# Optimization experiments

Hardware: AMD Instinct MI355X
Metric: run time of the kernel (lower is better)

## Reference

```python
import jax, jax.numpy as jnp
import numpy as np

EMB = 512
H1, H2 = 300, 100


def setup_inputs() -> dict:
    key = jax.random.key(0)
    ks = jax.random.split(key, 12)
    B, N, M = 2, 256, 256
    inp = {
        "action_embedding": jax.random.normal(ks[0], (B, EMB, N), jnp.float32),
        "anchor_embedding": jax.random.normal(ks[1], (B, EMB, M), jnp.float32),
        "action_points": jax.random.normal(ks[2], (B, 3, N), jnp.float32),
        "anchor_points": jax.random.normal(ks[3], (B, 3, M), jnp.float32),
        # MLPKernel params: Linear(1024,300), Linear(300,100), Linear(100,1), stored as [in,out]
        "W1": jax.random.normal(ks[4], (2 * EMB, H1), jnp.float32) / np.sqrt(2 * EMB),
        "b1": jax.random.normal(ks[5], (H1,), jnp.float32) * 0.01,
        "W2": jax.random.normal(ks[6], (H1, H2), jnp.float32) / np.sqrt(H1),
        "b2": jax.random.normal(ks[7], (H2,), jnp.float32) * 0.01,
        "W3": jax.random.normal(ks[8], (H2, 1), jnp.float32) / np.sqrt(H2),
        "b3": jax.random.normal(ks[9], (1,), jnp.float32) * 0.01,
    }
    return inp


def _pairwise_radii(Phi_A, Phi_B, W1, b1, W2, b2, W3, b3):
    # MLPKernel: softplus((mlp(cat(a,b)) + mlp(cat(b,a))) / 2) over all (n, m) pairs.
    # Split first linear: cat(x1,x2) @ W1 == x1 @ Wa + x2 @ Wb  (no [B,N,M,1024] materialization).
    F = Phi_A.shape[-1]
    Wa, Wb = W1[:F], W1[F:]
    hA_a = jnp.einsum('bnf,fh->bnh', Phi_A, Wa)
    hA_b = jnp.einsum('bnf,fh->bnh', Phi_A, Wb)
    hB_a = jnp.einsum('bmf,fh->bmh', Phi_B, Wa)
    hB_b = jnp.einsum('bmf,fh->bmh', Phi_B, Wb)

    def mlp_rest(h):  # h: [B,N,M,H1] pre-bias first-layer activations
        h = jax.nn.relu(h + b1)
        h = jax.nn.relu(jnp.einsum('bnmh,hk->bnmk', h, W2) + b2)
        return jnp.einsum('bnmk,ko->bnmo', h, W3) + b3

    v1 = mlp_rest(hA_a[:, :, None, :] + hB_b[:, None, :, :])  # mlp(cat(A_n, B_m))
    v2 = mlp_rest(hB_a[:, None, :, :] + hA_b[:, :, None, :])  # mlp(cat(B_m, A_n))
    return jax.nn.softplus((v1 + v2) * 0.5)[..., 0]  # [B,N,M]


def _multilaterate(P, R, W):
    # Vectorized estimate_p over batch b and query point n.
    # P: [B,M,3] anchor points, R: [B,N,M] estimated radii, W: [B,M] weights.
    M = P.shape[1]
    norm2 = jnp.sum(P * P, axis=-1)                      # [B,M]  (Pt @ P)
    d = norm2[:, None, :] - R ** 2                       # [B,N,M]  PtP - r^2
    a = jnp.einsum('bm,bnm,bmd->bnd', W, d, P) / M       # [B,N,3]
    WPPt = jnp.einsum('bm,bmd,bme->bde', W, P, P) / M    # [B,3,3]  mean(W * P Pt)
    mWd = jnp.einsum('bm,bnm->bn', W, d) / M             # [B,N]    mean(W * (PtP - r^2))
    c = jnp.einsum('bm,bmd->bd', W, P) / M               # [B,3]
    # B @ c with B = -2*mean(W*PPt) - mean(W*d)*I
    Bc = -2.0 * jnp.einsum('bde,be->bd', WPPt, c)[:, None, :] - mWd[..., None] * c[:, None, :]
    cc = jnp.sum(c * c, axis=-1)                         # [B]
    f = a + Bc + 2.0 * cc[:, None, None] * c[:, None, :]  # [B,N,3]
    PPt_mean = jnp.einsum('bmd,bme->bde', P, P) / M       # unweighted mean(PPt)
    H = -2.0 * PPt_mean + 2.0 * jnp.einsum('bd,be->bde', c, c)  # [B,3,3]
    Hinv = jnp.linalg.inv(H)
    q = -jnp.einsum('bde,bne->bnd', Hinv, f)
    return q + c[:, None, :]                              # [B,N,3]


def reference(action_embedding, anchor_embedding, action_points, anchor_points,
              W1, b1, W2, b2, W3, b3):
    P_A = jnp.transpose(action_points, (0, 2, 1))    # [B,N,3]
    P_B = jnp.transpose(anchor_points, (0, 2, 1))    # [B,M,3]
    Phi_A = jnp.transpose(action_embedding, (0, 2, 1))  # [B,N,F]
    Phi_B = jnp.transpose(anchor_embedding, (0, 2, 1))  # [B,M,F]
    B_weights = jnp.ones(Phi_B.shape[:2], dtype=Phi_B.dtype)
    R_est = _pairwise_radii(Phi_A, Phi_B, W1, b1, W2, b2, W3, b3)
    P_A_B_pred = _multilaterate(P_B, R_est, B_weights)  # [B,N,3]
    flow = jnp.transpose(P_A_B_pred - P_A, (0, 2, 1))   # [B,3,N] == full_flow (pred_weight=False)
    return flow
```

## Files before the change

kernel.cpp:

```cpp
#include <hip/hip_runtime.h>
#include <math.h>

#define EMB 512
#define H1 300
#define H2 100
#define NB 2
#define NN 256
#define MM 256

#define OFF_HAA 0
#define OFF_HAB (OFF_HAA + NB*NN*H1)
#define OFF_HBA (OFF_HAB + NB*NN*H1)
#define OFF_HBB (OFF_HBA + NB*NN*H1)
#define OFF_S   (OFF_HBB + NB*NN*H1)
#define OFF_CST (OFF_S + NB*NN*4)
#define OFF_W2C (OFF_CST + 64)
#define OFF_B2P (OFF_W2C + 17920)
#define OFF_W3P (OFF_B2P + 112)

typedef __attribute__((ext_vector_type(8))) short bf16x8;
typedef __attribute__((ext_vector_type(4))) float f32x4;

static __device__ inline unsigned f2bfbits(float f) {
    union { float f; unsigned u; } v; v.f = f;
    return (v.u + 0x7fffu + ((v.u >> 16) & 1u)) >> 16;
}

__global__ void k_prep(const float* __restrict__ W2, const float* __restrict__ b2,
                       const float* __restrict__ W3, float* __restrict__ ws)
{
    unsigned short* W2c = (unsigned short*)(ws + OFF_W2C);
    int start = blockIdx.x * 256 + threadIdx.x;
    for (int idx = start; idx < 10*112*32; idx += gridDim.x * 256) {
        int c  = idx / 3584;
        int r  = idx - c * 3584;
        int j  = r >> 5;
        int kk = r & 31;
        int k  = c * 32 + kk;
        float v = (j < H2 && k < H1) ? W2[k * H2 + j] : 0.0f;
        W2c[idx] = (unsigned short)f2bfbits(v);
    }
    if (blockIdx.x == 0 && threadIdx.x < 112) {
        int j = threadIdx.x;
        ws[OFF_B2P + j] = (j < H2) ? b2[j] : 0.0f;
        ws[OFF_W3P + j] = (j < H2) ? W3[j] : 0.0f;
    }
}

__global__ void k_const(const float* __restrict__ anchor_pts, float* __restrict__ cst)
{
    int b = blockIdx.x;
    int m = threadIdx.x;
    float px = anchor_pts[b*3*MM + 0*MM + m];
    float py = anchor_pts[b*3*MM + 1*MM + m];
    float pz = anchor_pts[b*3*MM + 2*MM + m];
    float n2 = px*px + py*py + pz*pz;

    float v[13];
    v[0]=px; v[1]=py; v[2]=pz;
    v[3]=px*px; v[4]=px*py; v[5]=px*pz; v[6]=py*py; v[7]=py*pz; v[8]=pz*pz;
    v[9]=n2*px; v[10]=n2*py; v[11]=n2*pz; v[12]=n2;

    #pragma unroll
    for (int off = 32; off >= 1; off >>= 1) {
        #pragma unroll
        for (int i = 0; i < 13; i++) v[i] += __shfl_xor(v[i], off, 64);
    }
    __shared__ float red[4][13];
    int wave = threadIdx.x >> 6, lane = threadIdx.x & 63;
    if (lane == 0) {
        #pragma unroll
        for (int i = 0; i < 13; i++) red[wave][i] = v[i];
    }
    __syncthreads();
    if (threadIdx.x == 0) {
        float s[13];
        #pragma unroll
        for (int i = 0; i < 13; i++)
            s[i] = red[0][i] + red[1][i] + red[2][i] + red[3][i];
        const float invM = 1.0f / MM;
        float c0 = s[0]*invM, c1 = s[1]*invM, c2 = s[2]*invM;
        float Pxx = s[3]*invM, Pxy = s[4]*invM, Pxz = s[5]*invM;
        float Pyy = s[6]*invM, Pyz = s[7]*invM, Pzz = s[8]*invM;

        float H00 = -2.0f*Pxx + 2.0f*c0*c0;
        float H01 = -2.0f*Pxy + 2.0f*c0*c1;
        float H02 = -2.0f*Pxz + 2.0f*c0*c2;
        float H11 = -2.0f*Pyy + 2.0f*c1*c1;
        float H12 = -2.0f*Pyz + 2.0f*c1*c2;
        float H22 = -2.0f*Pzz + 2.0f*c2*c2;
        float H10 = H01, H20 = H02, H21 = H12;

        float det = H00*(H11*H22 - H12*H21)
                  - H01*(H10*H22 - H12*H20)
                  + H02*(H10*H21 - H11*H20);
        float id = 1.0f / det;
        float i00 = (H11*H22 - H12*H21)*id;
        float i01 = (H02*H21 - H01*H22)*id;
        float i02 = (H01*H12 - H02*H11)*id;
        float i10 = (H12*H20 - H10*H22)*id;
        float i11 = (H00*H22 - H02*H20)*id;
        float i12 = (H02*H10 - H00*H12)*id;
        float i20 = (H10*H21 - H11*H20)*id;
        float i21 = (H01*H20 - H00*H21)*id;
        float i22 = (H00*H11 - H01*H10)*id;

        float t0x = -2.0f*(Pxx*c0 + Pxy*c1 + Pxz*c2);
        float t0y = -2.0f*(Pxy*c0 + Pyy*c1 + Pyz*c2);
        float t0z = -2.0f*(Pxz*c0 + Pyz*c1 + Pzz*c2);
        float cc = c0*c0 + c1*c1 + c2*c2;

        float* C = cst + b*32;
        C[0]=c0; C[1]=c1; C[2]=c2;
        C[3]=i00; C[4]=i01; C[5]=i02;
        C[6]=i10; C[7]=i11; C[8]=i12;
        C[9]=i20; C[10]=i21; C[11]=i22;
        C[12]=t0x; C[13]=t0y; C[14]=t0z;
        C[15]=cc;
        C[16]=s[9]*invM; C[17]=s[10]*invM; C[18]=s[11]*invM; C[19]=s[12]*invM;
    }
}

#define BN 64
#define BH 32
#define BK 32

__global__ __launch_bounds__(256) void k_hidden(
    const float* __restrict__ actE, const float* __restrict__ ancE,
    const float* __restrict__ W1, const float* __restrict__ b1,
    float* __restrict__ ws)
{
    int bs = blockIdx.z;
    int b = bs >> 1, src = bs & 1;
    int n0 = blockIdx.x * BN;
    int h0 = blockIdx.y * BH;
    const float* E = (src == 0 ? actE : ancE) + b * EMB * NN;
    float* outA = ws + (src == 0 ? OFF_HAA : OFF_HBA) + b * NN * H1;
    float* outB = ws + (src == 0 ? OFF_HAB : OFF_HBB) + b * NN * H1;

    __shared__ float Elds[BK][BN];
    __shared__ float Wlds[BK][BH];

    int tid = threadIdx.x;
    int tx = tid & 15;
    int ty = tid >> 4;

    float acc[4][2];
    #pragma unroll
    for (int i = 0; i < 4; i++) { acc[i][0] = 0.0f; acc[i][1] = 0.0f; }

    int ek  = tid >> 4;
    int en4 = (tid & 15) * 4;
    int wk  = tid >> 3;
    int wh4 = (tid & 7) * 4;
    int gh  = h0 + wh4;
    bool wvalid = (gh < 600);
    int whalf = (gh >= 300) ? 1 : 0;
    const float* wsrc = W1 + (size_t)whalf * EMB * H1 + (gh - whalf * 300);

    for (int k0 = 0; k0 < EMB; k0 += BK) {
        float4 e0 = *(const float4*)&E[(k0 + ek) * NN + n0 + en4];
        float4 e1 = *(const float4*)&E[(k0 + ek + 16) * NN + n0 + en4];
        float4 wv = make_float4(0.f, 0.f, 0.f, 0.f);
        if (wvalid) wv = *(const float4*)&wsrc[(size_t)(k0 + wk) * H1];

        __syncthreads();
        *(float4*)&Elds[ek][en4]      = e0;
        *(float4*)&Elds[ek + 16][en4] = e1;
        *(float4*)&Wlds[wk][wh4]      = wv;
        __syncthreads();

        #pragma unroll
        for (int k = 0; k < BK; k++) {
            float4 ev = *(const float4*)&Elds[k][ty * 4];
            float2 wv2 = *(const float2*)&Wlds[k][tx * 2];
            acc[0][0] = fmaf(ev.x, wv2.x, acc[0][0]);
            acc[0][1] = fmaf(ev.x, wv2.y, acc[0][1]);
            acc[1][0] = fmaf(ev.y, wv2.x, acc[1][0]);
            acc[1][1] = fmaf(ev.y, wv2.y, acc[1][1]);
            acc[2][0] = fmaf(ev.z, wv2.x, acc[2][0]);
            acc[2][1] = fmaf(ev.z, wv2.y, acc[2][1]);
            acc[3][0] = fmaf(ev.w, wv2.x, acc[3][0]);
            acc[3][1] = fmaf(ev.w, wv2.y, acc[3][1]);
        }
    }

    #pragma unroll
    for (int i = 0; i < 4; i++) {
        int n = n0 + ty * 4 + i;
        #pragma unroll
        for (int j = 0; j < 2; j++) {
            int h = h0 + tx * 2 + j;
            if (h < 600) {
                int hh = (h < 300) ? h : h - 300;
                float bias = (src == 0) ? b1[hh] : 0.0f;
                float val = acc[i][j] + bias;
                if (h < 300) outA[n * H1 + hh] = val;
                else         outB[n * H1 + hh] = val;
            }
        }
    }
}

__global__ __launch_bounds__(256, 2) void k_pair(
    const float* __restrict__ ws_f,
    const float* __restrict__ ancP,
    float* __restrict__ S)
{
    int b  = blockIdx.z;
    int n0 = blockIdx.y * 16, m0 = blockIdx.x * 16;
    int tid = threadIdx.x;
    int lane = tid & 63, w = tid >> 6;
    int colj = lane & 15;
    int quad = lane >> 4;

    __shared__ float hAfL[16 * 36];
    __shared__ float hBfL[16 * 36];
    __shared__ short Abf[256 * 40];
    __shared__ short W2L[112 * 40];

    const unsigned short* W2c = (const unsigned short*)(ws_f + OFF_W2C);
    const float* b2p = ws_f + OFF_B2P;
    const float* w3p = ws_f + OFF_W3P;

    float b2v[7], w3v[7];
    #pragma unroll
    for (int jt = 0; jt < 7; jt++) {
        b2v[jt] = b2p[jt * 16 + colj];
        w3v[jt] = w3p[jt * 16 + colj];
    }
    float pxv[4], pyv[4], pzv[4];
    #pragma unroll
    for (int r = 0; r < 4; r++) {
        int m = m0 + quad * 4 + r;
        pxv[r] = ancP[b*3*MM + 0*MM + m];
        pyv[r] = ancP[b*3*MM + 1*MM + m];
        pzv[r] = ancP[b*3*MM + 2*MM + m];
    }

    const float* Xb[2] = { ws_f + OFF_HAA + (size_t)(b*NN + n0) * H1,
                           ws_f + OFF_HAB + (size_t)(b*NN + n0) * H1 };
    const float* Yb[2] = { ws_f + OFF_HBB + (size_t)(b*NN + m0) * H1,
                           ws_f + OFF_HBA + (size_t)(b*NN + m0) * H1 };

    int sarr = tid >> 7;
    int srow = (tid >> 3) & 15;
    int sseg = tid & 7;
    int nl = tid >> 4, ml = tid & 15;

    float vsum[4][4];
    #pragma unroll
    for (int i = 0; i < 4; i++)
        #pragma unroll
        for (int r = 0; r < 4; r++) vsum[i][r] = 0.0f;

    #pragma unroll
    for (int p = 0; p < 2; p++) {
        f32x4 acc[4][7];
        #pragma unroll
        for (int i = 0; i < 4; i++)
            #pragma unroll
            for (int jt = 0; jt < 7; jt++)
                acc[i][jt] = (f32x4){0.f, 0.f, 0.f, 0.f};

        const float* Xp = Xb[p];
        const float* Yp = Yb[p];
        const float* ssrc = (sarr ? Yp : Xp) + srow * H1;

        for (int c = 0; c < 10; c++) {
            int k0 = c * 32;
            float4 sv = *(const float4*)&ssrc[k0 + sseg * 4];
            const uint4* wsrc4 = (const uint4*)W2c + c * 448;
            uint4 w0 = wsrc4[tid];
            uint4 w1 = wsrc4[(tid + 256) % 448];

            __syncthreads();
            {
                float* dst = (sarr ? hBfL : hAfL) + srow * 36 + sseg * 4;
                *(float4*)dst = sv;
            }
            {
                int j = tid >> 2, q = tid & 3;
                *(uint4*)&W2L[j * 40 + q * 8] = w0;
                if (tid < 192) {
                    int u2 = tid + 256;
                    int j2 = u2 >> 2, q2 = u2 & 3;
                    *(uint4*)&W2L[j2 * 40 + q2 * 8] = w1;
                }
            }
            __syncthreads();

            {
                const float* xa = hAfL + nl * 36;
                const float* xb = hBfL + ml * 36;
                short* arow = Abf + tid * 40;
                #pragma unroll
                for (int sg = 0; sg < 4; sg++) {
                    float4 a0 = *(const float4*)&xa[sg * 8];
                    float4 a1 = *(const float4*)&xa[sg * 8 + 4];
                    float4 c0 = *(const float4*)&xb[sg * 8];
                    float4 c1 = *(const float4*)&xb[sg * 8 + 4];
                    float h0 = fmaxf(a0.x + c0.x, 0.f);
                    float h1 = fmaxf(a0.y + c0.y, 0.f);
                    float h2 = fmaxf(a0.z + c0.z, 0.f);
                    float h3 = fmaxf(a0.w + c0.w, 0.f);
                    float h4 = fmaxf(a1.x + c1.x, 0.f);
                    float h5 = fmaxf(a1.y + c1.y, 0.f);
                    float h6 = fmaxf(a1.z + c1.z, 0.f);
                    float h7 = fmaxf(a1.w + c1.w, 0.f);
                    uint4 pk;
                    pk.x = f2bfbits(h0) | (f2bfbits(h1) << 16);
                    pk.y = f2bfbits(h2) | (f2bfbits(h3) << 16);
                    pk.z = f2bfbits(h4) | (f2bfbits(h5) << 16);
                    pk.w = f2bfbits(h6) | (f2bfbits(h7) << 16);
                    *(uint4*)&arow[sg * 8] = pk;
                }
            }
            __syncthreads();

            int koff = quad * 8;
            bf16x8 bfr[7];
            #pragma unroll
            for (int jt = 0; jt < 7; jt++)
                bfr[jt] = *(const bf16x8*)&W2L[(jt * 16 + colj) * 40 + koff];
            #pragma unroll
            for (int i = 0; i < 4; i++) {
                int pr = (w * 4 + i) * 16 + colj;
                bf16x8 af = *(const bf16x8*)&Abf[pr * 40 + koff];
                #pragma unroll
                for (int jt = 0; jt < 7; jt++)
                    acc[i][jt] = __builtin_amdgcn_mfma_f32_16x16x32_bf16(
                        af, bfr[jt], acc[i][jt], 0, 0, 0);
            }
        }

        #pragma unroll
        for (int i = 0; i < 4; i++)
            #pragma unroll
            for (int jt = 0; jt < 7; jt++)
                #pragma unroll
                for (int r = 0; r < 4; r++)
                    vsum[i][r] = fmaf(fmaxf(acc[i][jt][r] + b2v[jt], 0.f),
                                      w3v[jt], vsum[i][r]);
    }

    #pragma unroll
    for (int i = 0; i < 4; i++)
        #pragma unroll
        for (int r = 0; r < 4; r++) {
            float v = vsum[i][r];
            v += __shfl_xor(v, 1, 16);
            v += __shfl_xor(v, 2, 16);
            v += __shfl_xor(v, 4, 16);
            v += __shfl_xor(v, 8, 16);
            vsum[i][r] = v;
        }

    #pragma unroll
    for (int i = 0; i < 4; i++) {
        float s0 = 0.f, s1 = 0.f, s2 = 0.f, s3 = 0.f;
        #pragma unroll
        for (int r = 0; r < 4; r++) {
            float x = 0.5f * vsum[i][r];
            float R = fmaxf(x, 0.f) + log1pf(expf(-fabsf(x)));
            float r2 = R * R;
            s0 = fmaf(r2, pxv[r], s0);
            s1 = fmaf(r2, pyv[r], s1);
            s2 = fmaf(r2, pzv[r], s2);
            s3 += r2;
        }
        s0 += __shfl_xor(s0, 16, 64); s0 += __shfl_xor(s0, 32, 64);
        s1 += __shfl_xor(s1, 16, 64); s1 += __shfl_xor(s1, 32, 64);
        s2 += __shfl_xor(s2, 16, 64); s2 += __shfl_xor(s2, 32, 64);
        s3 += __shfl_xor(s3, 16, 64); s3 += __shfl_xor(s3, 32, 64);
        if (lane == 0) {
            int n = n0 + w * 4 + i;
            float* sp = S + (b*NN + n) * 4;
            atomicAdd(sp + 0, s0);
            atomicAdd(sp + 1, s1);
            atomicAdd(sp + 2, s2);
            atomicAdd(sp + 3, s3);
        }
    }
}

__global__ void k_final(const float* __restrict__ S, const float* __restrict__ cst,
                        const float* __restrict__ action_pts, float* __restrict__ out)
{
    int b = blockIdx.x;
    int n = threadIdx.x;
    const float* C = cst + b*32;
    float c0=C[0], c1=C[1], c2=C[2];
    float t0x=C[12], t0y=C[13], t0z=C[14];
    float cc=C[15];
    float SnP0=C[16], SnP1=C[17], SnP2=C[18], Sn=C[19];

    const float* sp = S + (b*NN + n) * 4;
    const float invM = 1.0f / MM;
    float a0 = SnP0 - sp[0]*invM;
    float a1 = SnP1 - sp[1]*invM;
    float a2 = SnP2 - sp[2]*invM;
    float mWd = Sn - sp[3]*invM;

    float f0 = a0 + t0x - mWd*c0 + 2.0f*cc*c0;
    float f1 = a1 + t0y - mWd*c1 + 2.0f*cc*c1;
    float f2 = a2 + t0z - mWd*c2 + 2.0f*cc*c2;

    float q0 = -(C[3]*f0 + C[4]*f1 + C[5]*f2);
    float q1 = -(C[6]*f0 + C[7]*f1 + C[8]*f2);
    float q2 = -(C[9]*f0 + C[10]*f1 + C[11]*f2);

    float p0 = q0 + c0, p1 = q1 + c1, p2 = q2 + c2;

    out[b*3*NN + 0*NN + n] = p0 - action_pts[b*3*NN + 0*NN + n];
    out[b*3*NN + 1*NN + n] = p1 - action_pts[b*3*NN + 1*NN + n];
    out[b*3*NN + 2*NN + n] = p2 - action_pts[b*3*NN + 2*NN + n];
}

extern "C" void kernel_launch(void* const* d_in, const int* in_sizes, int n_in,
                              void* d_out, int out_size, void* d_ws, size_t ws_size,
                              hipStream_t stream)
{
    const float* actE = (const float*)d_in[0];
    const float* ancE = (const float*)d_in[1];
    const float* actP = (const float*)d_in[2];
    const float* ancP = (const float*)d_in[3];
    const float* W1   = (const float*)d_in[4];
    const float* b1   = (const float*)d_in[5];
    const float* W2   = (const float*)d_in[6];
    const float* b2   = (const float*)d_in[7];
    const float* W3   = (const float*)d_in[8];
    const float* b3   = (const float*)d_in[9];
    float* ws  = (float*)d_ws;
    float* out = (float*)d_out;

    hipMemsetAsync(ws + OFF_S, 0, NB*NN*4*sizeof(float), stream);
    k_prep<<<16, 256, 0, stream>>>(W2, b2, W3, ws);
    k_const<<<NB, 256, 0, stream>>>(ancP, ws + OFF_CST);
    k_hidden<<<dim3(4, 19, 4), 256, 0, stream>>>(actE, ancE, W1, b1, ws);
    k_pair<<<dim3(16, 16, NB), 256, 0, stream>>>(ws, ancP, ws + OFF_S);
    k_final<<<NB, 256, 0, stream>>>(ws + OFF_S, ws + OFF_CST, actP, out);
}
```

Baseline: 155.6 us.

## Use bf16 MFMA for first layer, split pair kernel by permutation, add reduction kernel

Adds transpose-and-convert kernels for W1 and the embeddings to bf16, so the first-layer GEMM runs on MFMA instead of fp32 FMAs. The pair kernel is split across the two MLP permutations as separate grid slices. It builds the bf16 A-fragment directly in registers instead of staging it through shared memory, which removes an LDS buffer and a barrier. Per-pair logits are written to a workspace buffer and a new reduction kernel applies softplus and accumulates the multilateration sums, replacing the atomics and the memset. This adds kernel launches and extra global traffic, and lowers first-layer precision to bf16.

New measurement: 132.5 us. 1.17x faster.

```diff
diff --git a/kernel.cpp b/kernel.cpp
--- a/kernel.cpp
+++ b/kernel.cpp
@@ -1,4 +1,5 @@
 #include <hip/hip_runtime.h>
+#include <hip/hip_bf16.h>
 #include <math.h>
 
 #define EMB 512
@@ -9,14 +10,17 @@
 #define MM 256
 
 #define OFF_HAA 0
-#define OFF_HAB (OFF_HAA + NB*NN*H1)
-#define OFF_HBA (OFF_HAB + NB*NN*H1)
-#define OFF_HBB (OFF_HBA + NB*NN*H1)
-#define OFF_S   (OFF_HBB + NB*NN*H1)
-#define OFF_CST (OFF_S + NB*NN*4)
-#define OFF_W2C (OFF_CST + 64)
-#define OFF_B2P (OFF_W2C + 17920)
-#define OFF_W3P (OFF_B2P + 112)
+#define OFF_HAB 153600
+#define OFF_HBA 307200
+#define OFF_HBB 460800
+#define OFF_S   614400
+#define OFF_CST 616448
+#define OFF_W2C 616512
+#define OFF_B2P 634432
+#define OFF_W3P 634544
+#define OFF_ET  634656
+#define OFF_W1T 896800
+#define OFF_V   1060640
 
 typedef __attribute__((ext_vector_type(8))) short bf16x8;
 typedef __attribute__((ext_vector_type(4))) float f32x4;
@@ -24,6 +28,11 @@
 static __device__ inline unsigned f2bfbits(float f) {
     union { float f; unsigned u; } v; v.f = f;
     return (v.u + 0x7fffu + ((v.u >> 16) & 1u)) >> 16;
+}
+static __device__ inline unsigned pack_bf2(float a, float b) {
+    union { __hip_bfloat162 h; unsigned u; } cv;
+    cv.h = __float22bfloat162_rn(make_float2(a, b));
+    return cv.u;
 }
 
 __global__ void k_prep(const float* __restrict__ W2, const float* __restrict__ b2,
@@ -45,6 +54,53 @@
         ws[OFF_B2P + j] = (j < H2) ? b2[j] : 0.0f;
         ws[OFF_W3P + j] = (j < H2) ? W3[j] : 0.0f;
     }
+}
+
+__global__ void k_prepw1(const float* __restrict__ W1, float* __restrict__ ws)
+{
+    __shared__ float Tf[32 * 36];
+    unsigned short* W1t = (unsigned short*)(ws + OFF_W1T);
+    int h0 = blockIdx.x * 32, f0 = blockIdx.y * 32;
+    int tid = threadIdx.x;
+    int fr = tid >> 3, hc4 = (tid & 7) * 4;
+    int hg = h0 + hc4;
+    float4 v = make_float4(0.f, 0.f, 0.f, 0.f);
+    if (hg < 600) {
+        int half = (hg >= 300) ? 1 : 0;
+        int hh = hg - half * 300;
+        v = *(const float4*)&W1[(size_t)(half * EMB + f0 + fr) * H1 + hh];
+    }
+    *(float4*)&Tf[fr * 36 + hc4] = v;
+    __syncthreads();
+    int hr = tid >> 3, f4 = (tid & 7) * 4;
+    float v0 = Tf[(f4 + 0) * 36 + hr];
+    float v1 = Tf[(f4 + 1) * 36 + hr];
+    float v2 = Tf[(f4 + 2) * 36 + hr];
+    float v3 = Tf[(f4 + 3) * 36 + hr];
+    uint2 pk = make_uint2(pack_bf2(v0, v1), pack_bf2(v2, v3));
+    *(uint2*)&W1t[(size_t)(h0 + hr) * EMB + f0 + f4] = pk;
+}
+
+__global__ void k_prepe(const float* __restrict__ actE, const float* __restrict__ ancE,
+                        float* __restrict__ ws)
+{
+    __shared__ float Tf[32 * 36];
+    unsigned short* Et = (unsigned short*)(ws + OFF_ET);
+    int f0 = blockIdx.x * 32, n0 = blockIdx.y * 32;
+    int bs = blockIdx.z, b = bs >> 1, src = bs & 1;
+    const float* E = (src == 0 ? actE : ancE) + (size_t)b * EMB * NN;
+    int tid = threadIdx.x;
+    int r = tid >> 3, c4 = (tid & 7) * 4;
+    float4 v = *(const float4*)&E[(size_t)(f0 + r) * NN + n0 + c4];
+    *(float4*)&Tf[r * 36 + c4] = v;
+    __syncthreads();
+    int nr = tid >> 3, f4 = (tid & 7) * 4;
+    float v0 = Tf[(f4 + 0) * 36 + nr];
+    float v1 = Tf[(f4 + 1) * 36 + nr];
+    float v2 = Tf[(f4 + 2) * 36 + nr];
+    float v3 = Tf[(f4 + 3) * 36 + nr];
+    uint2 pk = make_uint2(pack_bf2(v0, v1), pack_bf2(v2, v3));
+    *(uint2*)&Et[((size_t)(bs * NN) + n0 + nr) * EMB + f0 + f4] = pk;
 }
 
 __global__ void k_const(const float* __restrict__ anchor_pts, float* __restrict__ cst)
@@ -121,228 +177,158 @@
     }
 }
 
-#define BN 64
-#define BH 32
-#define BK 32
-
 __global__ __launch_bounds__(256) void k_hidden(
-    const float* __restrict__ actE, const float* __restrict__ ancE,
-    const float* __restrict__ W1, const float* __restrict__ b1,
-    float* __restrict__ ws)
-{
-    int bs = blockIdx.z;
-    int b = bs >> 1, src = bs & 1;
-    int n0 = blockIdx.x * BN;
-    int h0 = blockIdx.y * BH;
-    const float* E = (src == 0 ? actE : ancE) + b * EMB * NN;
-    float* outA = ws + (src == 0 ? OFF_HAA : OFF_HBA) + b * NN * H1;
-    float* outB = ws + (src == 0 ? OFF_HAB : OFF_HBB) + b * NN * H1;
-
-    __shared__ float Elds[BK][BN];
-    __shared__ float Wlds[BK][BH];
+    float* __restrict__ ws, const float* __restrict__ b1)
+{
+    int bs = blockIdx.z, b = bs >> 1, src = bs & 1;
+    int n0 = blockIdx.x * 32;
+    int h0 = blockIdx.y * 64;
+    const unsigned short* Et  = (const unsigned short*)(ws + OFF_ET)
+                                + (size_t)(bs * NN) * EMB;
+    const unsigned short* W1t = (const unsigned short*)(ws + OFF_W1T);
+    float* outA = ws + (src == 0 ? OFF_HAA : OFF_HBA) + (size_t)b * NN * H1;
+    float* outB = ws + (src == 0 ? OFF_HAB : OFF_HBB) + (size_t)b * NN * H1;
+
+    __shared__ unsigned short EtL[32 * 40];
+    __shared__ unsigned short W1tL[64 * 40];
 
     int tid = threadIdx.x;
-    int tx = tid & 15;
-    int ty = tid >> 4;
-
-    float acc[4][2];
-    #pragma unroll
-    for (int i = 0; i < 4; i++) { acc[i][0] = 0.0f; acc[i][1] = 0.0f; }
-
-    int ek  = tid >> 4;
-    int en4 = (tid & 15) * 4;
-    int wk  = tid >> 3;
-    int wh4 = (tid & 7) * 4;
-    int gh  = h0 + wh4;
-    bool wvalid = (gh < 600);
-    int whalf = (gh >= 300) ? 1 : 0;
-    const float* wsrc = W1 + (size_t)whalf * EMB * H1 + (gh - whalf * 300);
-
-    for (int k0 = 0; k0 < EMB; k0 += BK) {
-        float4 e0 = *(const float4*)&E[(k0 + ek) * NN + n0 + en4];
-        float4 e1 = *(const float4*)&E[(k0 + ek + 16) * NN + n0 + en4];
-        float4 wv = make_float4(0.f, 0.f, 0.f, 0.f);
-        if (wvalid) wv = *(const float4*)&wsrc[(size_t)(k0 + wk) * H1];
-
+    int lane = tid & 63, w = tid >> 6;
+    int colj = lane & 15, quad = lane >> 4;
+    int pt = w & 1, jt0 = (w >> 1) * 2;
+
+    int erow = tid >> 3, es4 = (tid & 7) * 4;
+    int wrow = tid >> 2, ws8 = (tid & 3) * 8;
+
+    f32x4 acc[2];
+    acc[0] = (f32x4){0.f,0.f,0.f,0.f};
+    acc[1] = (f32x4){0.f,0.f,0.f,0.f};
+
+    for (int c = 0; c < 16; c++) {
+        int k0 = c * 32;
+        uint2 ev = *(const uint2*)&Et[(size_t)(n0 + erow) * EMB + k0 + es4];
+        uint4 wv = *(const uint4*)&W1t[(size_t)(h0 + wrow) * EMB + k0 + ws8];
         __syncthreads();
-        *(float4*)&Elds[ek][en4]      = e0;
-        *(float4*)&Elds[ek + 16][en4] = e1;
-        *(float4*)&Wlds[wk][wh4]      = wv;
+        *(uint2*)&EtL[erow * 40 + es4] = ev;
+        *(uint4*)&W1tL[wrow * 40 + ws8] = wv;
         __syncthreads();
 
-        #pragma unroll
-        for (int k = 0; k < BK; k++) {
-            float4 ev = *(const float4*)&Elds[k][ty * 4];
-            float2 wv2 = *(const float2*)&Wlds[k][tx * 2];
-            acc[0][0] = fmaf(ev.x, wv2.x, acc[0][0]);
-            acc[0][1] = fmaf(ev.x, wv2.y, acc[0][1]);
-            acc[1][0] = fmaf(ev.y, wv2.x, acc[1][0]);
-            acc[1][1] = fmaf(ev.y, wv2.y, acc[1][1]);
-            acc[2][0] = fmaf(ev.z, wv2.x, acc[2][0]);
-            acc[2][1] = fmaf(ev.z, wv2.y, acc[2][1]);
-            acc[3][0] = fmaf(ev.w, wv2.x, acc[3][0]);
-            acc[3][1] = fmaf(ev.w, wv2.y, acc[3][1]);
+        bf16x8 af  = *(const bf16x8*)&EtL[(pt * 16 + colj) * 40 + quad * 8];
+        bf16x8 bf0 = *(const bf16x8*)&W1tL[(jt0 * 16 + colj) * 40 + quad * 8];
+        bf16x8 bf1 = *(const bf16x8*)&W1tL[((jt0 + 1) * 16 + colj) * 40 + quad * 8];
+        acc[0] = __builtin_amdgcn_mfma_f32_16x16x32_bf16(af, bf0, acc[0], 0, 0, 0);
+        acc[1] = __builtin_amdgcn_mfma_f32_16x16x32_bf16(af, bf1, acc[1], 0, 0, 0);
+    }
+
+    #pragma unroll
+    for (int j2 = 0; j2 < 2; j2++) {
+        int hg = h0 + (jt0 + j2) * 16 + colj;
+        if (hg >= 600) continue;
+        int hh = (hg < 300) ? hg : hg - 300;
+        float* o = (hg < 300) ? outA : outB;
+        float bias = (src == 0) ? b1[hh] : 0.0f;
+        #pragma unroll
+        for (int r = 0; r < 4; r++) {
+            int n = n0 + pt * 16 + quad * 4 + r;
+            o[(size_t)n * H1 + hh] = acc[j2][r] + bias;
         }
     }
-
-    #pragma unroll
-    for (int i = 0; i < 4; i++) {
-        int n = n0 + ty * 4 + i;
-        #pragma unroll
-        for (int j = 0; j < 2; j++) {
-            int h = h0 + tx * 2 + j;
-            if (h < 600) {
-                int hh = (h < 300) ? h : h - 300;
-                float bias = (src == 0) ? b1[hh] : 0.0f;
-                float val = acc[i][j] + bias;
-                if (h < 300) outA[n * H1 + hh] = val;
-                else         outB[n * H1 + hh] = val;
-            }
-        }
-    }
-}
-
-__global__ __launch_bounds__(256, 2) void k_pair(
-    const float* __restrict__ ws_f,
-    const float* __restrict__ ancP,
-    float* __restrict__ S)
-{
-    int b  = blockIdx.z;
+}
+
+__global__ __launch_bounds__(256) void k_pair(
+    const float* __restrict__ ws_f, const float* __restrict__ b3p,
+    float* __restrict__ V)
+{
+    int bz = blockIdx.z, b = bz >> 1, p = bz & 1;
     int n0 = blockIdx.y * 16, m0 = blockIdx.x * 16;
     int tid = threadIdx.x;
     int lane = tid & 63, w = tid >> 6;
-    int colj = lane & 15;
-    int quad = lane >> 4;
+    int colj = lane & 15, quad = lane >> 4;
 
     __shared__ float hAfL[16 * 36];
     __shared__ float hBfL[16 * 36];
-    __shared__ short Abf[256 * 40];
     __shared__ short W2L[112 * 40];
 
     const unsigned short* W2c = (const unsigned short*)(ws_f + OFF_W2C);
-    const float* b2p = ws_f + OFF_B2P;
-    const float* w3p = ws_f + OFF_W3P;
-
     float b2v[7], w3v[7];
     #pragma unroll
     for (int jt = 0; jt < 7; jt++) {
-        b2v[jt] = b2p[jt * 16 + colj];
-        w3v[jt] = w3p[jt * 16 + colj];
-    }
-    float pxv[4], pyv[4], pzv[4];
-    #pragma unroll
-    for (int r = 0; r < 4; r++) {
-        int m = m0 + quad * 4 + r;
-        pxv[r] = ancP[b*3*MM + 0*MM + m];
-        pyv[r] = ancP[b*3*MM + 1*MM + m];
-        pzv[r] = ancP[b*3*MM + 2*MM + m];
-    }
-
-    const float* Xb[2] = { ws_f + OFF_HAA + (size_t)(b*NN + n0) * H1,
-                           ws_f + OFF_HAB + (size_t)(b*NN + n0) * H1 };
-    const float* Yb[2] = { ws_f + OFF_HBB + (size_t)(b*NN + m0) * H1,
-                           ws_f + OFF_HBA + (size_t)(b*NN + m0) * H1 };
+        b2v[jt] = ws_f[OFF_B2P + jt * 16 + colj];
+        w3v[jt] = ws_f[OFF_W3P + jt * 16 + colj];
+    }
+    float b3val = b3p[0];
+
+    const float* srcX = ws_f + (p == 0 ? OFF_HAA : OFF_HAB) + (size_t)(b*NN + n0) * H1;
+    const float* srcY = ws_f + (p == 0 ? OFF_HBB : OFF_HBA) + (size_t)(b*NN + m0) * H1;
 
     int sarr = tid >> 7;
     int srow = (tid >> 3) & 15;
     int sseg = tid & 7;
-    int nl = tid >> 4, ml = tid & 15;
-
-    float vsum[4][4];
+    const float* ssrc = (sarr ? srcY : srcX) + srow * H1;
+    float* sdst = (sarr ? hBfL : hAfL) + srow * 36 + sseg * 4;
+
+    f32x4 acc[4][7];
     #pragma unroll
     for (int i = 0; i < 4; i++)
         #pragma unroll
-        for (int r = 0; r < 4; r++) vsum[i][r] = 0.0f;
-
-    #pragma unroll
-    for (int p = 0; p < 2; p++) {
-        f32x4 acc[4][7];
-        #pragma unroll
-        for (int i = 0; i < 4; i++)
+        for (int jt = 0; jt < 7; jt++)
+            acc[i][jt] = (f32x4){0.f,0.f,0.f,0.f};
+
+    for (int c = 0; c < 10; c++) {
+        float4 sv = *(const float4*)&ssrc[c * 32 + sseg * 4];
+        const uint4* wsrc4 = (const uint4*)W2c + c * 448;
+        uint4 w0 = wsrc4[tid];
+        uint4 w1 = wsrc4[(tid + 256) % 448];
+
+        __syncthreads();
+        *(float4*)sdst = sv;
+        {
+            int j = tid >> 2, q = tid & 3;
+            *(uint4*)&W2L[j * 40 + q * 8] = w0;
+            if (tid < 192) {
+                int u2 = tid + 256;
+                *(uint4*)&W2L[(u2 >> 2) * 40 + (u2 & 3) * 8] = w1;
+            }
+        }
+        __syncthreads();
+
+        float4 hb0 = *(const float4*)&hBfL[colj * 36 + quad * 8];
+        float4 hb1 = *(const float4*)&hBfL[colj * 36 + quad * 8 + 4];
+        bf16x8 bfr[7];
+        #pragma unroll
+        for (int jt = 0; jt < 7; jt++)
+            bfr[jt] = *(const bf16x8*)&W2L[(jt * 16 + colj) * 40 + quad * 8];
+
+        #pragma unroll
+        for (int i = 0; i < 4; i++) {
+            const float* xa = &hAfL[(w * 4 + i) * 36 + quad * 8];
+            float4 ha0 = *(const float4*)&xa[0];
+            float4 ha1 = *(const float4*)&xa[4];
+            union { unsigned u[4]; bf16x8 v; } af;
+            af.u[0] = pack_bf2(fmaxf(ha0.x + hb0.x, 0.f), fmaxf(ha0.y + hb0.y, 0.f));
+            af.u[1] = pack_bf2(fmaxf(ha0.z + hb0.z, 0.f), fmaxf(ha0.w + hb0.w, 0.f));
+            af.u[2] = pack_bf2(fmaxf(ha1.x + hb1.x, 0.f), fmaxf(ha1.y + hb1.y, 0.f));
+            af.u[3] = pack_bf2(fmaxf(ha1.z + hb1.z, 0.f), fmaxf(ha1.w + hb1.w, 0.f));
             #pragma unroll
             for (int jt = 0; jt < 7; jt++)
-                acc[i][jt] = (f32x4){0.f, 0.f, 0.f, 0.f};
-
-        const float* Xp = Xb[p];
-        const float* Yp = Yb[p];
-        const float* ssrc = (sarr ? Yp : Xp) + srow * H1;
-
-        for (int c = 0; c < 10; c++) {
-            int k0 = c * 32;
-            float4 sv = *(const float4*)&ssrc[k0 + sseg * 4];
-            const uint4* wsrc4 = (const uint4*)W2c + c * 448;
-            uint4 w0 = wsrc4[tid];
-            uint4 w1 = wsrc4[(tid + 256) % 448];
-
-            __syncthreads();
-            {
-                float* dst = (sarr ? hBfL : hAfL) + srow * 36 + sseg * 4;
-                *(float4*)dst = sv;
-            }
-            {
-                int j = tid >> 2, q = tid & 3;
-                *(uint4*)&W2L[j * 40 + q * 8] = w0;
-                if (tid < 192) {
-                    int u2 = tid + 256;
-                    int j2 = u2 >> 2, q2 = u2 & 3;
-                    *(uint4*)&W2L[j2 * 40 + q2 * 8] = w1;
-                }
-            }
-            __syncthreads();
-
-            {
-                const float* xa = hAfL + nl * 36;
-                const float* xb = hBfL + ml * 36;
-                short* arow = Abf + tid * 40;
-                #pragma unroll
-                for (int sg = 0; sg < 4; sg++) {
-                    float4 a0 = *(const float4*)&xa[sg * 8];
-                    float4 a1 = *(const float4*)&xa[sg * 8 + 4];
-                    float4 c0 = *(const float4*)&xb[sg * 8];
-                    float4 c1 = *(const float4*)&xb[sg * 8 + 4];
-                    float h0 = fmaxf(a0.x + c0.x, 0.f);
-                    float h1 = fmaxf(a0.y + c0.y, 0.f);
-                    float h2 = fmaxf(a0.z + c0.z, 0.f);
-                    float h3 = fmaxf(a0.w + c0.w, 0.f);
-                    float h4 = fmaxf(a1.x + c1.x, 0.f);
-                    float h5 = fmaxf(a1.y + c1.y, 0.f);
-                    float h6 = fmaxf(a1.z + c1.z, 0.f);
-                    float h7 = fmaxf(a1.w + c1.w, 0.f);
-                    uint4 pk;
-                    pk.x = f2bfbits(h0) | (f2bfbits(h1) << 16);
-                    pk.y = f2bfbits(h2) | (f2bfbits(h3) << 16);
-                    pk.z = f2bfbits(h4) | (f2bfbits(h5) << 16);
-                    pk.w = f2bfbits(h6) | (f2bfbits(h7) << 16);
-                    *(uint4*)&arow[sg * 8] = pk;
-                }
-            }
-            __syncthreads();
-
-            int koff = quad * 8;
-            bf16x8 bfr[7];
+                acc[i][jt] = __builtin_amdgcn_mfma_f32_16x16x32_bf16(
+                    af.v, bfr[jt], acc[i][jt], 0, 0, 0);
+        }
+    }
+
+    float vsum[4][4];
+    #pragma unroll
+    for (int i = 0; i < 4; i++)
+        #pragma unroll
+        for (int r = 0; r < 4; r++) vsum[i][r] = 0.0f;
+    #pragma unroll
+    for (int i = 0; i < 4; i++)
+        #pragma unroll
+        for (int jt = 0; jt < 7; jt++)
             #pragma unroll
-            for (int jt = 0; jt < 7; jt++)
-                bfr[jt] = *(const bf16x8*)&W2L[(jt * 16 + colj) * 40 + koff];
-            #pragma unroll
-            for (int i = 0; i < 4; i++) {
-                int pr = (w * 4 + i) * 16 + colj;
-                bf16x8 af = *(const bf16x8*)&Abf[pr * 40 + koff];
-                #pragma unroll
-                for (int jt = 0; jt < 7; jt++)
-                    acc[i][jt] = __builtin_amdgcn_mfma_f32_16x16x32_bf16(
-                        af, bfr[jt], acc[i][jt], 0, 0, 0);
-            }
-        }
-
-        #pragma unroll
-        for (int i = 0; i < 4; i++)
-            #pragma unroll
-            for (int jt = 0; jt < 7; jt++)
-                #pragma unroll
-                for (int r = 0; r < 4; r++)
-                    vsum[i][r] = fmaf(fmaxf(acc[i][jt][r] + b2v[jt], 0.f),
-                                      w3v[jt], vsum[i][r]);
-    }
+            for (int r = 0; r < 4; r++)
+                vsum[i][r] = fmaf(fmaxf(acc[i][jt][r] + b2v[jt], 0.f),
+                                  w3v[jt], vsum[i][r]);
 
     #pragma unroll
     for (int i = 0; i < 4; i++)
@@ -356,31 +342,53 @@
             vsum[i][r] = v;
         }
 
-    #pragma unroll
-    for (int i = 0; i < 4; i++) {
-        float s0 = 0.f, s1 = 0.f, s2 = 0.f, s3 = 0.f;
-        #pragma unroll
-        for (int r = 0; r < 4; r++) {
-            float x = 0.5f * vsum[i][r];
-            float R = fmaxf(x, 0.f) + log1pf(expf(-fabsf(x)));
-            float r2 = R * R;
-            s0 = fmaf(r2, pxv[r], s0);
-            s1 = fmaf(r2, pyv[r], s1);
-            s2 = fmaf(r2, pzv[r], s2);
-            s3 += r2;
+    if (colj == 0) {
+        #pragma unroll
+        for (int i = 0; i < 4; i++) {
+            int n = n0 + w * 4 + i;
+            float4 o;
+            o.x = 0.5f * (vsum[i][0] + b3val);
+            o.y = 0.5f * (vsum[i][1] + b3val);
+            o.z = 0.5f * (vsum[i][2] + b3val);
+            o.w = 0.5f * (vsum[i][3] + b3val);
+            *(float4*)&V[(((size_t)p * NB + b) * NN + n) * MM + m0 + quad * 4] = o;
         }
-        s0 += __shfl_xor(s0, 16, 64); s0 += __shfl_xor(s0, 32, 64);
-        s1 += __shfl_xor(s1, 16, 64); s1 += __shfl_xor(s1, 32, 64);
-        s2 += __shfl_xor(s2, 16, 64); s2 += __shfl_xor(s2, 32, 64);
-        s3 += __shfl_xor(s3, 16, 64); s3 += __shfl_xor(s3, 32, 64);
-        if (lane == 0) {
-            int n = n0 + w * 4 + i;
-            float* sp = S + (b*NN + n) * 4;
-            atomicAdd(sp + 0, s0);
-            atomicAdd(sp + 1, s1);
-            atomicAdd(sp + 2, s2);
-            atomicAdd(sp + 3, s3);
-        }
+    }
+}
+
+__global__ void k_red(const float* __restrict__ V, const float* __restrict__ ancP,
+                      float* __restrict__ S)
+{
+    int b = blockIdx.y;
+    int n = blockIdx.x * 16 + (threadIdx.x >> 4);
+    int ml = threadIdx.x & 15;
+    const float* v0 = V + (((size_t)0 * NB + b) * NN + n) * MM;
+    const float* v1 = V + (((size_t)1 * NB + b) * NN + n) * MM;
+    float s0 = 0.f, s1 = 0.f, s2 = 0.f, s3 = 0.f;
+    #pragma unroll
+    for (int k = 0; k < 16; k++) {
+        int m = ml + k * 16;
+        float x = v0[m] + v1[m];
+        float R = fmaxf(x, 0.f) + log1pf(expf(-fabsf(x)));
+        float r2 = R * R;
+        float px = ancP[b*3*MM + 0*MM + m];
+        float py = ancP[b*3*MM + 1*MM + m];
+        float pz = ancP[b*3*MM + 2*MM + m];
+        s0 = fmaf(r2, px, s0);
+        s1 = fmaf(r2, py, s1);
+        s2 = fmaf(r2, pz, s2);
+        s3 += r2;
+    }
+    #pragma unroll
+    for (int off = 8; off >= 1; off >>= 1) {
+        s0 += __shfl_xor(s0, off, 16);
+        s1 += __shfl_xor(s1, off, 16);
+        s2 += __shfl_xor(s2, off, 16);
+        s3 += __shfl_xor(s3, off, 16);
+    }
+    if (ml == 0) {
+        float4 o = make_float4(s0, s1, s2, s3);
+        *(float4*)&S[(size_t)(b * NN + n) * 4] = o;
     }
 }
 
@@ -434,10 +442,12 @@
     float* ws  = (float*)d_ws;
     float* out = (float*)d_out;
 
-    hipMemsetAsync(ws + OFF_S, 0, NB*NN*4*sizeof(float), stream);
-    k_prep<<<16, 256, 0, stream>>>(W2, b2, W3, ws);
-    k_const<<<NB, 256, 0, stream>>>(ancP, ws + OFF_CST);
-    k_hidden<<<dim3(4, 19, 4), 256, 0, stream>>>(actE, ancE, W1, b1, ws);
-    k_pair<<<dim3(16, 16, NB), 256, 0, stream>>>(ws, ancP, ws + OFF_S);
-    k_final<<<NB, 256, 0, stream>>>(ws + OFF_S, ws + OFF_CST, actP, out);
-}
+    k_prep  <<<16, 256, 0, stream>>>(W2, b2, W3, ws);
+    k_prepw1<<<dim3(20, 16), 256, 0, stream>>>(W1, ws);
+    k_prepe <<<dim3(16, 8, 4), 256, 0, stream>>>(actE, ancE, ws);
+    k_const <<<NB, 256, 0, stream>>>(ancP, ws + OFF_CST);
+    k_hidden<<<dim3(8, 10, 4), 256, 0, stream>>>(ws, b1);
+    k_pair  <<<dim3(16, 16, NB*2), 256, 0, stream>>>(ws, b3, ws + OFF_V);
+    k_red   <<<dim3(16, NB), 256, 0, stream>>>(ws + OFF_V, ancP, ws + OFF_S);
+    k_final <<<NB, 256, 0, stream>>>(ws + OFF_S, ws + OFF_CST, actP, out);
+}
```
